# Kernel optimization log

Measured on AMD Instinct MI355X. Metric: run time of the kernel, lower is better.

The kernel has to match this reference:

```python
import jax, jax.numpy as jnp
import numpy as np

K = 1.0          # manifold curvature parameter (CustomLorentz k)
HEADS = 12
EPS = 1e-6


def add_time(space):
    """Lift space coords onto the hyperboloid: x0 = sqrt(k + ||x_s||^2)."""
    time = jnp.sqrt(K + jnp.sum(space * space, axis=-1, keepdims=True))
    return jnp.concatenate([time, space], axis=-1)


def lorentz_fc_heads(x, W):
    """LorentzFullyConnected with nheads: linear map, split space into heads,
    re-add per-head time coordinate. x: (b,n,F) -> (b,h,n,hd+1)."""
    y = x @ W                                   # (b, n, F)
    b, n, _ = y.shape
    space = y[..., 1:].reshape(b, n, HEADS, -1).transpose(0, 2, 1, 3)  # (b,h,n,hd)
    return add_time(space)


def pairwise_csqdist(q, k):
    """Lorentzian squared distance d^2(x,y) = -2k - 2<x,y>_L, pairwise."""
    inner_space = jnp.einsum('bhid,bhjd->bhij', q[..., 1:], k[..., 1:])
    inner_time = q[..., 0][..., :, None] * k[..., 0][..., None, :]
    inner = inner_space - inner_time            # Lorentz inner product
    return jnp.maximum(-2.0 * K - 2.0 * inner, EPS)


def centroid(v, w):
    """Lorentz centroid: m = w @ v; c = sqrt(k) * m / sqrt(|<m,m>_L|)."""
    m = jnp.einsum('bhij,bhjd->bhid', w, v)     # (b,h,n,hd+1)
    li = jnp.sum(m[..., 1:] ** 2, axis=-1, keepdims=True) - m[..., :1] ** 2
    denom = jnp.sqrt(jnp.maximum(jnp.abs(li), EPS))
    return jnp.sqrt(K) * m / denom


def setup_inputs() -> dict:
    key = jax.random.key(0)
    ks = jax.random.split(key, 5)
    b, n, f = 8, 1024, 769
    x_space = jax.random.normal(ks[0], (b, n, f - 1), dtype=jnp.float32) * 0.5
    x = add_time(x_space)                       # valid hyperboloid points
    init = 0.02
    Wq = jax.random.normal(ks[1], (f, f), dtype=jnp.float32) * init
    Wk = jax.random.normal(ks[2], (f, f), dtype=jnp.float32) * init
    Wv = jax.random.normal(ks[3], (f, f), dtype=jnp.float32) * init
    Wo = jax.random.normal(ks[4], (f, f), dtype=jnp.float32) * init
    return {"x": x, "Wq": Wq, "Wk": Wk, "Wv": Wv, "Wo": Wo}


def reference(x, Wq, Wk, Wv, Wo):
    b, n, _ = x.shape
    q = lorentz_fc_heads(x, Wq)                 # (b,h,n,hd+1)
    k = lorentz_fc_heads(x, Wk)
    v = lorentz_fc_heads(x, Wv)

    d2 = pairwise_csqdist(q, k)                 # (b,h,n,n)
    # score: softmax over query axis (-2) of 1/(1+log(1+d2)), then transpose
    score = jax.nn.softmax(1.0 / (1.0 + jnp.log1p(d2)), axis=-2)
    score = jnp.swapaxes(score, -1, -2)         # rows now sum to 1 over last dim

    attn = centroid(v, score)                   # (b,h,n,hd+1)

    attn_space = attn[..., 1:].transpose(0, 2, 1, 3).reshape(b, n, -1)  # (b,n,h*hd)
    attn_time = attn[..., 0].transpose(0, 2, 1)                         # (b,n,h)
    time_r = jnp.sqrt(jnp.maximum(
        jnp.sum(attn_time ** 2, axis=-1, keepdims=True) - (HEADS - 1) * K, EPS))
    merged = jnp.concatenate([time_r, attn_space], axis=-1)             # (b,n,F)

    # output LorentzFullyConnected (single-head, normalize=False, no dropout at eval)
    y = merged @ Wo
    return add_time(y[..., 1:])
```

## Files before the change

### kernel.cpp

```cpp
#include <hip/hip_runtime.h>
#include <hip/hip_bf16.h>
#include <math.h>

#define HEADS 12
#define NSEQ 1024
#define BATCH 8
#define FDIM 769
#define KP 800
#define NROWS (BATCH*NSEQ)
#define BH (BATCH*HEADS)
#define BHROWS (BH*NSEQ)

typedef __attribute__((ext_vector_type(8))) short bf16x8_t;
typedef __attribute__((ext_vector_type(4))) short bf16x4_t;
typedef __attribute__((ext_vector_type(4))) float f32x4_t;

__device__ __forceinline__ unsigned short f2bf(float f){
    unsigned u = __float_as_uint(f);
    return (unsigned short)((u + 0x7FFFu + ((u >> 16) & 1u)) >> 16);
}

__device__ __forceinline__ float fast_rcp(float x){
    return __builtin_amdgcn_rcpf(x);
}
__device__ __forceinline__ float fast_exp2(float x){
    return __builtin_amdgcn_exp2f(x);
}
__device__ __forceinline__ float fast_log2(float x){
    return __builtin_amdgcn_logf(x);
}

__global__ __launch_bounds__(256) void conv_x(const float* __restrict__ x, ushort* __restrict__ xb){
    int idx = blockIdx.x*256 + threadIdx.x;
    int r = idx / 200, c4 = (idx % 200) * 4;
    const float* row = x + (size_t)r * FDIM;
    ushort4 o;
    o.x = (c4+0 < FDIM) ? f2bf(row[c4+0]) : (ushort)0;
    o.y = (c4+1 < FDIM) ? f2bf(row[c4+1]) : (ushort)0;
    o.z = (c4+2 < FDIM) ? f2bf(row[c4+2]) : (ushort)0;
    o.w = (c4+3 < FDIM) ? f2bf(row[c4+3]) : (ushort)0;
    *(ushort4*)(xb + (size_t)r*KP + c4) = o;
}

__global__ __launch_bounds__(256) void conv_w(const float* __restrict__ Wq, const float* __restrict__ Wk,
                                              const float* __restrict__ Wv, const float* __restrict__ Wo,
                                              ushort* __restrict__ WcatT, ushort* __restrict__ WoT){
    int kt = blockIdx.x, nt = blockIdx.y, mat = blockIdx.z;
    const float* W = (mat==0)?Wq:(mat==1)?Wk:(mat==2)?Wv:Wo;
    __shared__ float T[32][33];
    int t = threadIdx.x;
    #pragma unroll
    for (int p=0; p<4; p++){
        int idx = t + p*256;
        int kk = idx>>5, nn = idx&31;
        int kp = kt*32 + kk;
        int srck;
        if (mat < 3) srck = (kp < FDIM) ? kp : -1;
        else         srck = (kp < 768) ? kp+1 : ((kp==768) ? 0 : -1);
        T[kk][nn] = (srck >= 0) ? W[(size_t)srck*FDIM + (nt*32+nn) + 1] : 0.0f;
    }
    __syncthreads();
    ushort* outp = (mat < 3) ? (WcatT + (size_t)mat*768*KP) : WoT;
    #pragma unroll
    for (int p=0; p<4; p++){
        int idx = t + p*256;
        int nl = idx>>5, kk = idx&31;
        outp[(size_t)(nt*32+nl)*KP + kt*32 + kk] = f2bf(T[kk][nl]);
    }
}

__global__ __launch_bounds__(256) void gemm_qkv(const ushort* __restrict__ A, const ushort* __restrict__ Bt,
                                                ushort* __restrict__ qkv, float* __restrict__ tbuf){
    __shared__ __align__(16) ushort As[2][128*32];
    __shared__ __align__(16) ushort Bs[2][128*32];
    const int m0 = blockIdx.x*128, n0 = blockIdx.y*128;
    const int tid = threadIdx.x, lane = tid&63, wave = tid>>6;
    const int wm = wave>>1, wn = wave&1;
    const int g = lane>>4, c = lane&15;

    f32x4_t acc[4][4];
    #pragma unroll
    for (int i=0;i<4;i++)
        #pragma unroll
        for (int j=0;j<4;j++) acc[i][j] = (f32x4_t){0.f,0.f,0.f,0.f};

    bf16x8_t ra[2], rb[2];
    auto LOADS = [&](int kt){
        int k0 = kt*32;
        #pragma unroll
        for (int p=0;p<2;p++){
            int idx = tid + p*256;
            int row = idx>>2, ch = idx&3;
            ra[p] = *(const bf16x8_t*)(A  + (size_t)(m0+row)*KP + k0 + ch*8);
            rb[p] = *(const bf16x8_t*)(Bt + (size_t)(n0+row)*KP + k0 + ch*8);
        }
    };
    auto WRITES = [&](int buf){
        #pragma unroll
        for (int p=0;p<2;p++){
            int idx = tid + p*256;
            int row = idx>>2, ch = idx&3;
            int sw = (ch ^ (row&3))*8;
            *(bf16x8_t*)&As[buf][row*32 + sw] = ra[p];
            *(bf16x8_t*)&Bs[buf][row*32 + sw] = rb[p];
        }
    };

    LOADS(0); WRITES(0); __syncthreads();
    for (int kt=0; kt<25; kt++){
        int cur = kt&1;
        if (kt+1 < 25) LOADS(kt+1);
        bf16x8_t af[4], bf[4];
        #pragma unroll
        for (int mf=0; mf<4; mf++){
            int row = wm*64 + mf*16 + c;
            af[mf] = *(const bf16x8_t*)&As[cur][row*32 + ((g ^ (row&3))*8)];
        }
        #pragma unroll
        for (int nf=0; nf<4; nf++){
            int row = wn*64 + nf*16 + c;
            bf[nf] = *(const bf16x8_t*)&Bs[cur][row*32 + ((g ^ (row&3))*8)];
        }
        #pragma unroll
        for (int mf=0; mf<4; mf++)
            #pragma unroll
            for (int nf=0; nf<4; nf++)
                acc[mf][nf] = __builtin_amdgcn_mfma_f32_16x16x32_bf16(af[mf], bf[nf], acc[mf][nf], 0,0,0);
        if (kt+1 < 25) WRITES(cur^1);
        __syncthreads();
    }

    const int nb = n0 + wn*64;
    const int matv = nb / 768;
    const int hh = (nb % 768) / 64;
    #pragma unroll
    for (int mf=0; mf<4; mf++){
        #pragma unroll
        for (int j=0; j<4; j++){
            int m = m0 + wm*64 + mf*16 + g*4 + j;
            int bb = m >> 10, ns = m & (NSEQ-1);
            size_t rowidx = ((size_t)bb*HEADS + hh)*NSEQ + ns;
            size_t sbase = (size_t)matv*((size_t)BHROWS*64) + rowidx*64;
            float sum = 0.f;
            #pragma unroll
            for (int nf=0; nf<4; nf++){
                float v = acc[mf][nf][j];
                qkv[sbase + nf*16 + c] = f2bf(v);
                sum += v*v;
            }
            sum += __shfl_xor(sum,1,64); sum += __shfl_xor(sum,2,64);
            sum += __shfl_xor(sum,4,64); sum += __shfl_xor(sum,8,64);
            if (c == 0) tbuf[(size_t)matv*BHROWS + rowidx] = sqrtf(1.0f + sum);
        }
    }
}

__global__ __launch_bounds__(256) void transpose_v(const ushort* __restrict__ vsp, ushort* __restrict__ vT){
    const int bh = blockIdx.x >> 3, it128 = blockIdx.x & 7;
    __shared__ ushort T2[64*136];
    const int tid = threadIdx.x;
    {
        int ii = tid>>1, half = tid&1;
        const ushort* src = vsp + ((size_t)bh*NSEQ + it128*128 + ii)*64 + half*32;
        bf16x8_t rr[4];
        #pragma unroll
        for (int p=0;p<4;p++) rr[p] = *(const bf16x8_t*)(src + p*8);
        #pragma unroll
        for (int p=0;p<4;p++)
            #pragma unroll
            for (int e=0;e<8;e++)
                T2[(half*32 + p*8 + e)*136 + ii] = (ushort)rr[p][e];
    }
    __syncthreads();
    {
        int dd = tid>>2, qq = tid&3;
        ushort* dst = vT + ((size_t)bh*64 + dd)*NSEQ + it128*128 + qq*32;
        #pragma unroll
        for (int p=0;p<4;p++)
            *(bf16x8_t*)(dst + p*8) = *(const bf16x8_t*)&T2[dd*136 + qq*32 + p*8];
    }
}

__global__ __launch_bounds__(256, 4) void lorentz_attn(
    const ushort* __restrict__ qsp, const ushort* __restrict__ ksp, const ushort* __restrict__ vT,
    const float* __restrict__ qtg, const float* __restrict__ ktg, const float* __restrict__ vtg,
    ushort* __restrict__ merged, float* __restrict__ ct)
{
    const int lin = blockIdx.x;
    const int bh = lin % BH;
    const int jt = lin / BH;
    const int b = bh / HEADS, h = bh % HEADS;
    const size_t rb = (size_t)bh * NSEQ;

    __shared__ __align__(16) ushort QVbuf[2][9216];
    __shared__ __align__(16) float qts[2][64];
    __shared__ __align__(16) float kts[128];

    const int tid = threadIdx.x, lane = tid&63, wave = tid>>6;
    const int g = lane>>4, c = lane&15;

    ushort* Kst = &QVbuf[0][0];

    bf16x8_t rq[2], rv[2]; float rqt = 0.f, rvt = 0.f;
    const int ii = tid>>2, qc = tid&3;
    auto LOADQV = [&](int it){
        int i0 = it*64;
        const ushort* qp = qsp + (rb + i0 + ii)*64 + qc*16;
        rq[0] = *(const bf16x8_t*)(qp);
        rq[1] = *(const bf16x8_t*)(qp + 8);
        const ushort* vp = vT + ((size_t)bh*64 + ii)*NSEQ + i0 + qc*16;
        rv[0] = *(const bf16x8_t*)(vp);
        rv[1] = *(const bf16x8_t*)(vp + 8);
        if (tid < 64) rqt = qtg[rb + i0 + tid];
        else if (tid < 128) rvt = vtg[rb + i0 + (tid-64)];
    };
    auto WRITEQV = [&](int buf){
        ushort* Qb = &QVbuf[buf][0];
        ushort* Vb = &QVbuf[buf][4096];
        *(bf16x8_t*)&Qb[ii*64 + (((2*qc  ) ^ (ii&7))*8)] = rq[0];
        *(bf16x8_t*)&Qb[ii*64 + (((2*qc+1) ^ (ii&7))*8)] = rq[1];
        #pragma unroll
        for (int s=0; s<4; s++){
            bf16x4_t sl = (s&1) ? (bf16x4_t)__builtin_shufflevector(rv[s>>1], rv[s>>1], 4,5,6,7)
                                : (bf16x4_t)__builtin_shufflevector(rv[s>>1], rv[s>>1], 0,1,2,3);
            *(bf16x4_t*)&Vb[ii*64 + ((qc*16 + s*4) ^ ((ii&7)<<2))] = sl;
        }
        if (tid < 64) qts[buf][tid] = rqt;
        else if (tid < 128) Vb[64*64 + (tid-64)] = f2bf(rvt);
    };

    LOADQV(0);
    {
        int row = tid>>1, half = tid&1;
        const ushort* kp = ksp + (rb + jt*128 + row)*64 + half*32;
        bf16x8_t kr[4];
        #pragma unroll
        for (int p=0;p<4;p++) kr[p] = *(const bf16x8_t*)(kp + p*8);
        #pragma unroll
        for (int p=0;p<4;p++){
            int c8 = half*4 + p;
            *(bf16x8_t*)&Kst[row*64 + ((c8 ^ (row&7))*8)] = kr[p];
        }
    }
    if (tid < 128) kts[tid] = ktg[rb + jt*128 + tid];
    for (int idx = tid; idx < 2*15*64; idx += 256){
        int bz = idx/(15*64), r2 = idx%(15*64);
        QVbuf[bz][4096 + (65 + (r2>>6))*64 + (r2&63)] = 0;
    }
    __syncthreads();

    bf16x8_t kfrag[2][2]; float kt2[2];
    #pragma unroll
    for (int jf=0; jf<2; jf++){
        int row = wave*32 + jf*16 + c;
        #pragma unroll
        for (int kc=0; kc<2; kc++)
            kfrag[jf][kc] = *(const bf16x8_t*)&Kst[row*64 + (((kc*4+g) ^ (row&7))*8)];
        kt2[jf] = 2.0f * kts[row];
    }
    __syncthreads();
    WRITEQV(0);
    __syncthreads();

    f32x4_t acc[2][5];
    #pragma unroll
    for (int jf=0; jf<2; jf++)
        #pragma unroll
        for (int dt=0; dt<5; dt++) acc[jf][dt] = (f32x4_t){0.f,0.f,0.f,0.f};

    for (int it=0; it<16; it++){
        int cur = it&1;
        if (it+1 < 16) LOADQV(it+1);
        ushort* Qc = &QVbuf[cur][0];
        ushort* Vc = &QVbuf[cur][4096];
        #pragma unroll
        for (int ib=0; ib<4; ib++){
            int qrow = ib*16 + c;
            bf16x8_t qf0 = *(const bf16x8_t*)&Qc[qrow*64 + (((  g) ^ (qrow&7))*8)];
            bf16x8_t qf1 = *(const bf16x8_t*)&Qc[qrow*64 + (((4+g) ^ (qrow&7))*8)];
            f32x4_t qt4 = *(const f32x4_t*)&qts[cur][ib*16 + g*4];
            bf16x4_t vf[5];
            #pragma unroll
            for (int dt=0; dt<5; dt++){
                int d = dt*16 + c;
                vf[dt] = *(const bf16x4_t*)&Vc[d*64 + ((ib*16 + g*4) ^ ((d&7)<<2))];
            }
            #pragma unroll
            for (int jf=0; jf<2; jf++){
                f32x4_t dacc = (f32x4_t){0.f,0.f,0.f,0.f};
                dacc = __builtin_amdgcn_mfma_f32_16x16x32_bf16(qf0, kfrag[jf][0], dacc, 0,0,0);
                dacc = __builtin_amdgcn_mfma_f32_16x16x32_bf16(qf1, kfrag[jf][1], dacc, 0,0,0);
                float w[4];
                #pragma unroll
                for (int r=0; r<4; r++){
                    float c0 = fmaf(qt4[r], kt2[jf], -1.0f);
                    float t  = fmaf(-2.0f, dacc[r], c0);
                    t = fmaxf(t, 1.000001f);
                    float L  = fast_log2(t);
                    float u  = fmaf(0.69314718056f, L, 1.0f);
                    w[r] = fast_exp2(fast_rcp(u) * 1.44269504089f);
                }
                __hip_bfloat162 h01 = __float22bfloat162_rn(float2{w[0], w[1]});
                __hip_bfloat162 h23 = __float22bfloat162_rn(float2{w[2], w[3]});
                union { __hip_bfloat162 h2[2]; bf16x4_t v4; } uu;
                uu.h2[0] = h01; uu.h2[1] = h23;
                bf16x4_t pa = uu.v4;
                __builtin_amdgcn_s_setprio(1);
                #pragma unroll
                for (int dt=0; dt<5; dt++)
                    acc[jf][dt] = __builtin_amdgcn_mfma_f32_16x16x16bf16_1k(pa, vf[dt], acc[jf][dt], 0,0,0);
                __builtin_amdgcn_s_setprio(0);
            }
        }
        if (it+1 < 16) WRITEQV(cur^1);
        __syncthreads();
    }

    ushort* Ms = &QVbuf[0][0];
    #pragma unroll
    for (int jf=0; jf<2; jf++){
        #pragma unroll
        for (int r=0; r<4; r++){
            float part = 0.f;
            #pragma unroll
            for (int dt=0; dt<4; dt++) part += acc[jf][dt][r]*acc[jf][dt][r];
            part += __shfl_xor(part,1,64); part += __shfl_xor(part,2,64);
            part += __shfl_xor(part,4,64); part += __shfl_xor(part,8,64);
            float tv = acc[jf][4][r];
            float tb = __shfl(tv, lane & 48, 64);
            float li = part - tb*tb;
            float f = rsqrtf(fmaxf(fabsf(li), 1e-6f));
            int jl = wave*32 + jf*16 + g*4 + r;
            #pragma unroll
            for (int dt=0; dt<4; dt++)
                Ms[jl*64 + dt*16 + c] = f2bf(acc[jf][dt][r]*f);
            if (c == 0)
                ct[((size_t)b*NSEQ + jt*128 + jl)*HEADS + h] = tb*f;
        }
    }
    __syncthreads();
    {
        int row = tid>>1, half = tid&1;
        size_t gb = ((size_t)b*NSEQ + jt*128 + row)*KP + h*64 + half*32;
        #pragma unroll
        for (int q4=0; q4<4; q4++)
            *(bf16x8_t*)(merged + gb + q4*8) = *(const bf16x8_t*)&Ms[row*64 + half*32 + q4*8];
    }
}

__global__ __launch_bounds__(256) void gemm_out_k(const ushort* __restrict__ A, const ushort* __restrict__ Bt,
                                                  float* __restrict__ out){
    __shared__ __align__(16) ushort As[2][128*32];
    __shared__ __align__(16) ushort Bs[2][128*32];
    const int m0 = blockIdx.x*128, n0 = blockIdx.y*128;
    const int tid = threadIdx.x, lane = tid&63, wave = tid>>6;
    const int wm = wave>>1, wn = wave&1;
    const int g = lane>>4, c = lane&15;

    f32x4_t acc[4][4];
    #pragma unroll
    for (int i=0;i<4;i++)
        #pragma unroll
        for (int j=0;j<4;j++) acc[i][j] = (f32x4_t){0.f,0.f,0.f,0.f};

    bf16x8_t ra[2], rb[2];
    auto LOADS = [&](int kt){
        int k0 = kt*32;
        #pragma unroll
        for (int p=0;p<2;p++){
            int idx = tid + p*256;
            int row = idx>>2, ch = idx&3;
            ra[p] = *(const bf16x8_t*)(A  + (size_t)(m0+row)*KP + k0 + ch*8);
            rb[p] = *(const bf16x8_t*)(Bt + (size_t)(n0+row)*KP + k0 + ch*8);
        }
    };
    auto WRITES = [&](int buf){
        #pragma unroll
        for (int p=0;p<2;p++){
            int idx = tid + p*256;
            int row = idx>>2, ch = idx&3;
            int sw = (ch ^ (row&3))*8;
            *(bf16x8_t*)&As[buf][row*32 + sw] = ra[p];
            *(bf16x8_t*)&Bs[buf][row*32 + sw] = rb[p];
        }
    };

    LOADS(0); WRITES(0); __syncthreads();
    for (int kt=0; kt<25; kt++){
        int cur = kt&1;
        if (kt+1 < 25) LOADS(kt+1);
        bf16x8_t af[4], bf[4];
        #pragma unroll
        for (int mf=0; mf<4; mf++){
            int row = wm*64 + mf*16 + c;
            af[mf] = *(const bf16x8_t*)&As[cur][row*32 + ((g ^ (row&3))*8)];
        }
        #pragma unroll
        for (int nf=0; nf<4; nf++){
            int row = wn*64 + nf*16 + c;
            bf[nf] = *(const bf16x8_t*)&Bs[cur][row*32 + ((g ^ (row&3))*8)];
        }
        #pragma unroll
        for (int mf=0; mf<4; mf++)
            #pragma unroll
            for (int nf=0; nf<4; nf++)
                acc[mf][nf] = __builtin_amdgcn_mfma_f32_16x16x32_bf16(af[mf], bf[nf], acc[mf][nf], 0,0,0);
        if (kt+1 < 25) WRITES(cur^1);
        __syncthreads();
    }

    #pragma unroll
    for (int mf=0; mf<4; mf++){
        #pragma unroll
        for (int j=0; j<4; j++){
            int m = m0 + wm*64 + mf*16 + g*4 + j;
            #pragma unroll
            for (int nf=0; nf<4; nf++)
                out[(size_t)m*FDIM + 1 + n0 + wn*64 + nf*16 + c] = acc[mf][nf][j];
        }
    }
}

__global__ __launch_bounds__(256) void zero_pad(ushort* __restrict__ merged){
    int idx = blockIdx.x*256 + threadIdx.x;
    int r = idx>>5, cc = idx&31;
    if (cc > 0) merged[(size_t)r*KP + 768 + cc] = 0;
}

__global__ __launch_bounds__(256) void time_r_k(const float* __restrict__ ct, ushort* __restrict__ merged){
    int r = blockIdx.x*256 + threadIdx.x;
    float s = 0.f;
    #pragma unroll
    for (int hh=0; hh<HEADS; hh++){
        float t = ct[(size_t)r*HEADS + hh];
        s = fmaf(t, t, s);
    }
    merged[(size_t)r*KP + 768] = f2bf(sqrtf(fmaxf(s - (float)(HEADS-1), 1e-6f)));
}

__global__ __launch_bounds__(256) void out_time(float* __restrict__ out)
{
    int row = blockIdx.x*4 + (threadIdx.x>>6);
    int lane = threadIdx.x & 63;
    float s = 0.f;
    #pragma unroll
    for (int l=0; l<12; l++){
        float v = out[(size_t)row*FDIM + 1 + lane + l*64];
        s = fmaf(v, v, s);
    }
    #pragma unroll
    for (int off=32; off; off>>=1) s += __shfl_down(s, off, 64);
    if (lane == 0) out[(size_t)row*FDIM] = sqrtf(1.0f + s);
}

extern "C" void kernel_launch(void* const* d_in, const int* in_sizes, int n_in,
                              void* d_out, int out_size, void* d_ws, size_t ws_size,
                              hipStream_t stream)
{
    const float* x  = (const float*)d_in[0];
    const float* Wq = (const float*)d_in[1];
    const float* Wk = (const float*)d_in[2];
    const float* Wv = (const float*)d_in[3];
    const float* Wo = (const float*)d_in[4];
    float* out = (float*)d_out;

    char* p = (char*)d_ws;
    ushort* xb     = (ushort*)p; p += (size_t)NROWS*KP*2;
    ushort* WcatT  = (ushort*)p; p += (size_t)2304*KP*2;
    ushort* WoT    = (ushort*)p; p += (size_t)768*KP*2;
    ushort* qkv    = (ushort*)p; p += (size_t)3*BHROWS*64*2;
    float*  tbuf   = (float*)p;  p += (size_t)3*BHROWS*4;
    float*  ct     = (float*)p;  p += (size_t)NROWS*HEADS*4;
    ushort* merged = (ushort*)p; p += (size_t)NROWS*KP*2;
    ushort* vT     = (ushort*)p; p += (size_t)BH*64*NSEQ*2;

    const size_t SP = (size_t)BHROWS*64;

    conv_x<<<6400, 256, 0, stream>>>(x, xb);
    conv_w<<<dim3(25,24,4), 256, 0, stream>>>(Wq, Wk, Wv, Wo, WcatT, WoT);
    gemm_qkv<<<dim3(64,18), 256, 0, stream>>>(xb, WcatT, qkv, tbuf);
    transpose_v<<<768, 256, 0, stream>>>(qkv + 2*SP, vT);
    zero_pad<<<1024, 256, 0, stream>>>(merged);
    lorentz_attn<<<768, 256, 0, stream>>>(qkv, qkv + SP, vT,
                                          tbuf, tbuf + BHROWS, tbuf + 2*BHROWS,
                                          merged, ct);
    time_r_k<<<NROWS/256, 256, 0, stream>>>(ct, merged);
    gemm_out_k<<<dim3(64,6), 256, 0, stream>>>(merged, WoT, out);
    out_time<<<NROWS/4, 256, 0, stream>>>(out);
}
```

Before: 179.2 us.

## Split attention keys across more waves, approximate log via float bits, fuse pad zeroing

The attention kernel now runs 512 threads per block, so each wave owns 16 keys instead of 32. This halves per-thread accumulators and frees registers for more resident waves. The hardware log2 is replaced by a bit-cast (Mitchell-style) log2 approximation with the constants folded in, and the lower clamp on the distance term is dropped. The separate zero_pad kernel is removed and its padding writes are merged into time_r_k. The log approximation has an absolute error of up to about 0.09 in log2, which perturbs the softmax weights and risks accuracy.

```diff
diff --git a/kernel.cpp b/kernel.cpp
--- a/kernel.cpp
+++ b/kernel.cpp
@@ -25,9 +25,6 @@
 }
 __device__ __forceinline__ float fast_exp2(float x){
     return __builtin_amdgcn_exp2f(x);
-}
-__device__ __forceinline__ float fast_log2(float x){
-    return __builtin_amdgcn_logf(x);
 }
 
 __global__ __launch_bounds__(256) void conv_x(const float* __restrict__ x, ushort* __restrict__ xb){
@@ -181,7 +178,7 @@
     }
 }
 
-__global__ __launch_bounds__(256, 4) void lorentz_attn(
+__global__ __launch_bounds__(512, 6) void lorentz_attn(
     const ushort* __restrict__ qsp, const ushort* __restrict__ ksp, const ushort* __restrict__ vT,
     const float* __restrict__ qtg, const float* __restrict__ ktg, const float* __restrict__ vtg,
     ushort* __restrict__ merged, float* __restrict__ ct)
@@ -201,72 +198,57 @@
 
     ushort* Kst = &QVbuf[0][0];
 
-    bf16x8_t rq[2], rv[2]; float rqt = 0.f, rvt = 0.f;
-    const int ii = tid>>2, qc = tid&3;
+    bf16x8_t rq, rv; float rqt = 0.f, rvt = 0.f;
+    const int srow = tid>>3, sch = tid&7;
     auto LOADQV = [&](int it){
         int i0 = it*64;
-        const ushort* qp = qsp + (rb + i0 + ii)*64 + qc*16;
-        rq[0] = *(const bf16x8_t*)(qp);
-        rq[1] = *(const bf16x8_t*)(qp + 8);
-        const ushort* vp = vT + ((size_t)bh*64 + ii)*NSEQ + i0 + qc*16;
-        rv[0] = *(const bf16x8_t*)(vp);
-        rv[1] = *(const bf16x8_t*)(vp + 8);
+        rq = *(const bf16x8_t*)(qsp + (rb + i0 + srow)*64 + sch*8);
+        rv = *(const bf16x8_t*)(vT + ((size_t)bh*64 + srow)*NSEQ + i0 + sch*8);
         if (tid < 64) rqt = qtg[rb + i0 + tid];
         else if (tid < 128) rvt = vtg[rb + i0 + (tid-64)];
     };
     auto WRITEQV = [&](int buf){
         ushort* Qb = &QVbuf[buf][0];
         ushort* Vb = &QVbuf[buf][4096];
-        *(bf16x8_t*)&Qb[ii*64 + (((2*qc  ) ^ (ii&7))*8)] = rq[0];
-        *(bf16x8_t*)&Qb[ii*64 + (((2*qc+1) ^ (ii&7))*8)] = rq[1];
-        #pragma unroll
-        for (int s=0; s<4; s++){
-            bf16x4_t sl = (s&1) ? (bf16x4_t)__builtin_shufflevector(rv[s>>1], rv[s>>1], 4,5,6,7)
-                                : (bf16x4_t)__builtin_shufflevector(rv[s>>1], rv[s>>1], 0,1,2,3);
-            *(bf16x4_t*)&Vb[ii*64 + ((qc*16 + s*4) ^ ((ii&7)<<2))] = sl;
-        }
+        *(bf16x8_t*)&Qb[srow*64 + ((sch ^ (srow&7))*8)] = rq;
+        bf16x4_t lo = __builtin_shufflevector(rv, rv, 0,1,2,3);
+        bf16x4_t hi = __builtin_shufflevector(rv, rv, 4,5,6,7);
+        *(bf16x4_t*)&Vb[srow*64 + ((sch*8    ) ^ ((srow&7)<<2))] = lo;
+        *(bf16x4_t*)&Vb[srow*64 + ((sch*8 + 4) ^ ((srow&7)<<2))] = hi;
         if (tid < 64) qts[buf][tid] = rqt;
         else if (tid < 128) Vb[64*64 + (tid-64)] = f2bf(rvt);
     };
 
     LOADQV(0);
     {
-        int row = tid>>1, half = tid&1;
-        const ushort* kp = ksp + (rb + jt*128 + row)*64 + half*32;
-        bf16x8_t kr[4];
-        #pragma unroll
-        for (int p=0;p<4;p++) kr[p] = *(const bf16x8_t*)(kp + p*8);
-        #pragma unroll
-        for (int p=0;p<4;p++){
-            int c8 = half*4 + p;
-            *(bf16x8_t*)&Kst[row*64 + ((c8 ^ (row&7))*8)] = kr[p];
-        }
+        int row = tid>>2, kc16 = tid&3;
+        const ushort* kp = ksp + (rb + jt*128 + row)*64 + kc16*16;
+        bf16x8_t k0 = *(const bf16x8_t*)(kp);
+        bf16x8_t k1 = *(const bf16x8_t*)(kp + 8);
+        *(bf16x8_t*)&Kst[row*64 + (((kc16*2  ) ^ (row&7))*8)] = k0;
+        *(bf16x8_t*)&Kst[row*64 + (((kc16*2+1) ^ (row&7))*8)] = k1;
     }
     if (tid < 128) kts[tid] = ktg[rb + jt*128 + tid];
-    for (int idx = tid; idx < 2*15*64; idx += 256){
+    for (int idx = tid; idx < 2*15*64; idx += 512){
         int bz = idx/(15*64), r2 = idx%(15*64);
         QVbuf[bz][4096 + (65 + (r2>>6))*64 + (r2&63)] = 0;
     }
     __syncthreads();
 
-    bf16x8_t kfrag[2][2]; float kt2[2];
-    #pragma unroll
-    for (int jf=0; jf<2; jf++){
-        int row = wave*32 + jf*16 + c;
-        #pragma unroll
-        for (int kc=0; kc<2; kc++)
-            kfrag[jf][kc] = *(const bf16x8_t*)&Kst[row*64 + (((kc*4+g) ^ (row&7))*8)];
-        kt2[jf] = 2.0f * kts[row];
+    bf16x8_t kfrag[2]; float kt2e;
+    {
+        int krow = wave*16 + c;
+        kfrag[0] = *(const bf16x8_t*)&Kst[krow*64 + (((  g) ^ (krow&7))*8)];
+        kfrag[1] = *(const bf16x8_t*)&Kst[krow*64 + (((4+g) ^ (krow&7))*8)];
+        kt2e = 5.43656365691809f * kts[krow];
     }
     __syncthreads();
     WRITEQV(0);
     __syncthreads();
 
-    f32x4_t acc[2][5];
-    #pragma unroll
-    for (int jf=0; jf<2; jf++)
-        #pragma unroll
-        for (int dt=0; dt<5; dt++) acc[jf][dt] = (f32x4_t){0.f,0.f,0.f,0.f};
+    f32x4_t acc[5];
+    #pragma unroll
+    for (int dt=0; dt<5; dt++) acc[dt] = (f32x4_t){0.f,0.f,0.f,0.f};
 
     for (int it=0; it<16; it++){
         int cur = it&1;
@@ -285,32 +267,27 @@
                 int d = dt*16 + c;
                 vf[dt] = *(const bf16x4_t*)&Vc[d*64 + ((ib*16 + g*4) ^ ((d&7)<<2))];
             }
-            #pragma unroll
-            for (int jf=0; jf<2; jf++){
-                f32x4_t dacc = (f32x4_t){0.f,0.f,0.f,0.f};
-                dacc = __builtin_amdgcn_mfma_f32_16x16x32_bf16(qf0, kfrag[jf][0], dacc, 0,0,0);
-                dacc = __builtin_amdgcn_mfma_f32_16x16x32_bf16(qf1, kfrag[jf][1], dacc, 0,0,0);
-                float w[4];
-                #pragma unroll
-                for (int r=0; r<4; r++){
-                    float c0 = fmaf(qt4[r], kt2[jf], -1.0f);
-                    float t  = fmaf(-2.0f, dacc[r], c0);
-                    t = fmaxf(t, 1.000001f);
-                    float L  = fast_log2(t);
-                    float u  = fmaf(0.69314718056f, L, 1.0f);
-                    w[r] = fast_exp2(fast_rcp(u) * 1.44269504089f);
-                }
-                __hip_bfloat162 h01 = __float22bfloat162_rn(float2{w[0], w[1]});
-                __hip_bfloat162 h23 = __float22bfloat162_rn(float2{w[2], w[3]});
-                union { __hip_bfloat162 h2[2]; bf16x4_t v4; } uu;
-                uu.h2[0] = h01; uu.h2[1] = h23;
-                bf16x4_t pa = uu.v4;
-                __builtin_amdgcn_s_setprio(1);
-                #pragma unroll
-                for (int dt=0; dt<5; dt++)
-                    acc[jf][dt] = __builtin_amdgcn_mfma_f32_16x16x16bf16_1k(pa, vf[dt], acc[jf][dt], 0,0,0);
-                __builtin_amdgcn_s_setprio(0);
+            f32x4_t dacc = (f32x4_t){0.f,0.f,0.f,0.f};
+            dacc = __builtin_amdgcn_mfma_f32_16x16x32_bf16(qf0, kfrag[0], dacc, 0,0,0);
+            dacc = __builtin_amdgcn_mfma_f32_16x16x32_bf16(qf1, kfrag[1], dacc, 0,0,0);
+            float w[4];
+            #pragma unroll
+            for (int r=0; r<4; r++){
+                float c0e = fmaf(qt4[r], kt2e, -2.718281828f);
+                float s   = fmaf(dacc[r], -5.43656365691809f, c0e);
+                float L   = fmaf((float)__float_as_int(s), 0x1p-23f, -126.9570f);
+                w[r] = fast_exp2(fast_rcp(L) * 2.08136898f);
             }
+            __hip_bfloat162 h01 = __float22bfloat162_rn(float2{w[0], w[1]});
+            __hip_bfloat162 h23 = __float22bfloat162_rn(float2{w[2], w[3]});
+            union { __hip_bfloat162 h2[2]; bf16x4_t v4; } uu;
+            uu.h2[0] = h01; uu.h2[1] = h23;
+            bf16x4_t pa = uu.v4;
+            __builtin_amdgcn_s_setprio(1);
+            #pragma unroll
+            for (int dt=0; dt<5; dt++)
+                acc[dt] = __builtin_amdgcn_mfma_f32_16x16x16bf16_1k(pa, vf[dt], acc[dt], 0,0,0);
+            __builtin_amdgcn_s_setprio(0);
         }
         if (it+1 < 16) WRITEQV(cur^1);
         __syncthreads();
@@ -318,33 +295,29 @@
 
     ushort* Ms = &QVbuf[0][0];
     #pragma unroll
-    for (int jf=0; jf<2; jf++){
-        #pragma unroll
-        for (int r=0; r<4; r++){
-            float part = 0.f;
-            #pragma unroll
-            for (int dt=0; dt<4; dt++) part += acc[jf][dt][r]*acc[jf][dt][r];
-            part += __shfl_xor(part,1,64); part += __shfl_xor(part,2,64);
-            part += __shfl_xor(part,4,64); part += __shfl_xor(part,8,64);
-            float tv = acc[jf][4][r];
-            float tb = __shfl(tv, lane & 48, 64);
-            float li = part - tb*tb;
-            float f = rsqrtf(fmaxf(fabsf(li), 1e-6f));
-            int jl = wave*32 + jf*16 + g*4 + r;
-            #pragma unroll
-            for (int dt=0; dt<4; dt++)
-                Ms[jl*64 + dt*16 + c] = f2bf(acc[jf][dt][r]*f);
-            if (c == 0)
-                ct[((size_t)b*NSEQ + jt*128 + jl)*HEADS + h] = tb*f;
-        }
+    for (int r=0; r<4; r++){
+        float part = 0.f;
+        #pragma unroll
+        for (int dt=0; dt<4; dt++) part += acc[dt][r]*acc[dt][r];
+        part += __shfl_xor(part,1,64); part += __shfl_xor(part,2,64);
+        part += __shfl_xor(part,4,64); part += __shfl_xor(part,8,64);
+        float tv = acc[4][r];
+        float tb = __shfl(tv, lane & 48, 64);
+        float li = part - tb*tb;
+        float f = rsqrtf(fmaxf(fabsf(li), 1e-6f));
+        int jl = wave*16 + g*4 + r;
+        #pragma unroll
+        for (int dt=0; dt<4; dt++)
+            Ms[jl*64 + dt*16 + c] = f2bf(acc[dt][r]*f);
+        if (c == 0)
+            ct[((size_t)b*NSEQ + jt*128 + jl)*HEADS + h] = tb*f;
     }
     __syncthreads();
     {
-        int row = tid>>1, half = tid&1;
-        size_t gb = ((size_t)b*NSEQ + jt*128 + row)*KP + h*64 + half*32;
-        #pragma unroll
-        for (int q4=0; q4<4; q4++)
-            *(bf16x8_t*)(merged + gb + q4*8) = *(const bf16x8_t*)&Ms[row*64 + half*32 + q4*8];
+        int row = tid>>2, q16 = tid&3;
+        size_t gb = ((size_t)b*NSEQ + jt*128 + row)*KP + h*64 + q16*16;
+        *(bf16x8_t*)(merged + gb)     = *(const bf16x8_t*)&Ms[row*64 + q16*16];
+        *(bf16x8_t*)(merged + gb + 8) = *(const bf16x8_t*)&Ms[row*64 + q16*16 + 8];
     }
 }
 
@@ -421,12 +394,6 @@
     }
 }
 
-__global__ __launch_bounds__(256) void zero_pad(ushort* __restrict__ merged){
-    int idx = blockIdx.x*256 + threadIdx.x;
-    int r = idx>>5, cc = idx&31;
-    if (cc > 0) merged[(size_t)r*KP + 768 + cc] = 0;
-}
-
 __global__ __launch_bounds__(256) void time_r_k(const float* __restrict__ ct, ushort* __restrict__ merged){
     int r = blockIdx.x*256 + threadIdx.x;
     float s = 0.f;
@@ -435,7 +402,14 @@
         float t = ct[(size_t)r*HEADS + hh];
         s = fmaf(t, t, s);
     }
-    merged[(size_t)r*KP + 768] = f2bf(sqrtf(fmaxf(s - (float)(HEADS-1), 1e-6f)));
+    bf16x8_t z = (bf16x8_t){0,0,0,0,0,0,0,0};
+    bf16x8_t z0 = z;
+    z0[0] = (short)f2bf(sqrtf(fmaxf(s - (float)(HEADS-1), 1e-6f)));
+    ushort* dst = merged + (size_t)r*KP + 768;
+    *(bf16x8_t*)(dst)      = z0;
+    *(bf16x8_t*)(dst + 8)  = z;
+    *(bf16x8_t*)(dst + 16) = z;
+    *(bf16x8_t*)(dst + 24) = z;
 }
 
 __global__ __launch_bounds__(256) void out_time(float* __restrict__ out)
@@ -480,8 +454,7 @@
     conv_w<<<dim3(25,24,4), 256, 0, stream>>>(Wq, Wk, Wv, Wo, WcatT, WoT);
     gemm_qkv<<<dim3(64,18), 256, 0, stream>>>(xb, WcatT, qkv, tbuf);
     transpose_v<<<768, 256, 0, stream>>>(qkv + 2*SP, vT);
-    zero_pad<<<1024, 256, 0, stream>>>(merged);
-    lorentz_attn<<<768, 256, 0, stream>>>(qkv, qkv + SP, vT,
+    lorentz_attn<<<768, 512, 0, stream>>>(qkv, qkv + SP, vT,
                                           tbuf, tbuf + BHROWS, tbuf + 2*BHROWS,
                                           merged, ct);
     time_r_k<<<NROWS/256, 256, 0, stream>>>(ct, merged);
```

Measured after the change: 172.8 us. -3.6%, faster.

## Use bit-trick log approximation, wider PV MFMA, and fold zero_pad into time_r

Applied to the files above, without the earlier changes.

Swaps the log2 in the score transform for an integer-reinterpretation log approximation with rescaled constants, which removes one transcendental per score. Two query sub-blocks are now processed per iteration so the P·V product can use the 16x16x32 MFMA with 8-wide fragments; this needed a new V tile swizzle and a permuted time-row layout. The separate zero_pad launch is removed and time_r_k writes the padded row with vector stores. Launch bounds drop to 3 waves per SIMD to leave room for more registers. The bit-trick log is a coarse approximation, so accuracy on the score path may suffer.

```diff
diff --git a/kernel.cpp b/kernel.cpp
--- a/kernel.cpp
+++ b/kernel.cpp
@@ -25,9 +25,6 @@
 }
 __device__ __forceinline__ float fast_exp2(float x){
     return __builtin_amdgcn_exp2f(x);
-}
-__device__ __forceinline__ float fast_log2(float x){
-    return __builtin_amdgcn_logf(x);
 }
 
 __global__ __launch_bounds__(256) void conv_x(const float* __restrict__ x, ushort* __restrict__ xb){
@@ -181,7 +178,7 @@
     }
 }
 
-__global__ __launch_bounds__(256, 4) void lorentz_attn(
+__global__ __launch_bounds__(256, 3) void lorentz_attn(
     const ushort* __restrict__ qsp, const ushort* __restrict__ ksp, const ushort* __restrict__ vT,
     const float* __restrict__ qtg, const float* __restrict__ ktg, const float* __restrict__ vtg,
     ushort* __restrict__ merged, float* __restrict__ ct)
@@ -202,13 +199,13 @@
     ushort* Kst = &QVbuf[0][0];
 
     bf16x8_t rq[2], rv[2]; float rqt = 0.f, rvt = 0.f;
-    const int ii = tid>>2, qc = tid&3;
+    const int sr = tid>>2, sch = tid&3;
     auto LOADQV = [&](int it){
         int i0 = it*64;
-        const ushort* qp = qsp + (rb + i0 + ii)*64 + qc*16;
+        const ushort* qp = qsp + (rb + i0 + sr)*64 + sch*16;
         rq[0] = *(const bf16x8_t*)(qp);
         rq[1] = *(const bf16x8_t*)(qp + 8);
-        const ushort* vp = vT + ((size_t)bh*64 + ii)*NSEQ + i0 + qc*16;
+        const ushort* vp = vT + ((size_t)bh*64 + sr)*NSEQ + i0 + sch*16;
         rv[0] = *(const bf16x8_t*)(vp);
         rv[1] = *(const bf16x8_t*)(vp + 8);
         if (tid < 64) rqt = qtg[rb + i0 + tid];
@@ -217,29 +214,33 @@
     auto WRITEQV = [&](int buf){
         ushort* Qb = &QVbuf[buf][0];
         ushort* Vb = &QVbuf[buf][4096];
-        *(bf16x8_t*)&Qb[ii*64 + (((2*qc  ) ^ (ii&7))*8)] = rq[0];
-        *(bf16x8_t*)&Qb[ii*64 + (((2*qc+1) ^ (ii&7))*8)] = rq[1];
+        *(bf16x8_t*)&Qb[sr*64 + (((2*sch  ) ^ (sr&7))*8)] = rq[0];
+        *(bf16x8_t*)&Qb[sr*64 + (((2*sch+1) ^ (sr&7))*8)] = rq[1];
+        int pbase = (sch>>1)*32 + (sch&1)*4;
+        int sx = (sr&7)*8;
         #pragma unroll
         for (int s=0; s<4; s++){
             bf16x4_t sl = (s&1) ? (bf16x4_t)__builtin_shufflevector(rv[s>>1], rv[s>>1], 4,5,6,7)
                                 : (bf16x4_t)__builtin_shufflevector(rv[s>>1], rv[s>>1], 0,1,2,3);
-            *(bf16x4_t*)&Vb[ii*64 + ((qc*16 + s*4) ^ ((ii&7)<<2))] = sl;
+            *(bf16x4_t*)&Vb[sr*64 + ((pbase + 8*s) ^ sx)] = sl;
         }
         if (tid < 64) qts[buf][tid] = rqt;
-        else if (tid < 128) Vb[64*64 + (tid-64)] = f2bf(rvt);
+        else if (tid < 128){
+            int i = tid - 64;
+            int p = 32*(i>>5) + 8*((i>>2)&3) + 4*((i>>4)&1) + (i&3);
+            Vb[64*64 + p] = f2bf(rvt);
+        }
     };
 
     LOADQV(0);
     {
         int row = tid>>1, half = tid&1;
         const ushort* kp = ksp + (rb + jt*128 + row)*64 + half*32;
-        bf16x8_t kr[4];
-        #pragma unroll
-        for (int p=0;p<4;p++) kr[p] = *(const bf16x8_t*)(kp + p*8);
-        #pragma unroll
-        for (int p=0;p<4;p++){
+        #pragma unroll
+        for (int p=0; p<4; p++){
+            bf16x8_t kr = *(const bf16x8_t*)(kp + p*8);
             int c8 = half*4 + p;
-            *(bf16x8_t*)&Kst[row*64 + ((c8 ^ (row&7))*8)] = kr[p];
+            *(bf16x8_t*)&Kst[row*64 + ((c8 ^ (row&7))*8)] = kr;
         }
     }
     if (tid < 128) kts[tid] = ktg[rb + jt*128 + tid];
@@ -249,14 +250,13 @@
     }
     __syncthreads();
 
-    bf16x8_t kfrag[2][2]; float kt2[2];
+    bf16x8_t kfrag[2][2]; float kt2e[2];
     #pragma unroll
     for (int jf=0; jf<2; jf++){
-        int row = wave*32 + jf*16 + c;
-        #pragma unroll
-        for (int kc=0; kc<2; kc++)
-            kfrag[jf][kc] = *(const bf16x8_t*)&Kst[row*64 + (((kc*4+g) ^ (row&7))*8)];
-        kt2[jf] = 2.0f * kts[row];
+        int krow = wave*32 + jf*16 + c;
+        kfrag[jf][0] = *(const bf16x8_t*)&Kst[krow*64 + (((  g) ^ (krow&7))*8)];
+        kfrag[jf][1] = *(const bf16x8_t*)&Kst[krow*64 + (((4+g) ^ (krow&7))*8)];
+        kt2e[jf] = 5.43656365691809f * kts[krow];
     }
     __syncthreads();
     WRITEQV(0);
@@ -274,41 +274,52 @@
         ushort* Qc = &QVbuf[cur][0];
         ushort* Vc = &QVbuf[cur][4096];
         #pragma unroll
-        for (int ib=0; ib<4; ib++){
-            int qrow = ib*16 + c;
-            bf16x8_t qf0 = *(const bf16x8_t*)&Qc[qrow*64 + (((  g) ^ (qrow&7))*8)];
-            bf16x8_t qf1 = *(const bf16x8_t*)&Qc[qrow*64 + (((4+g) ^ (qrow&7))*8)];
-            f32x4_t qt4 = *(const f32x4_t*)&qts[cur][ib*16 + g*4];
-            bf16x4_t vf[5];
+        for (int ib2=0; ib2<2; ib2++){
+            bf16x8_t qf[2][2];
+            #pragma unroll
+            for (int t=0; t<2; t++){
+                int qrow = ib2*32 + t*16 + c;
+                qf[t][0] = *(const bf16x8_t*)&Qc[qrow*64 + (((  g) ^ (qrow&7))*8)];
+                qf[t][1] = *(const bf16x8_t*)&Qc[qrow*64 + (((4+g) ^ (qrow&7))*8)];
+            }
+            f32x4_t qt0 = *(const f32x4_t*)&qts[cur][ib2*32 + g*4];
+            f32x4_t qt1 = *(const f32x4_t*)&qts[cur][ib2*32 + 16 + g*4];
+            bf16x8_t vf[5];
             #pragma unroll
             for (int dt=0; dt<5; dt++){
                 int d = dt*16 + c;
-                vf[dt] = *(const bf16x4_t*)&Vc[d*64 + ((ib*16 + g*4) ^ ((d&7)<<2))];
+                vf[dt] = *(const bf16x8_t*)&Vc[d*64 + ((ib2*32 + g*8) ^ ((d&7)*8))];
             }
             #pragma unroll
             for (int jf=0; jf<2; jf++){
-                f32x4_t dacc = (f32x4_t){0.f,0.f,0.f,0.f};
-                dacc = __builtin_amdgcn_mfma_f32_16x16x32_bf16(qf0, kfrag[jf][0], dacc, 0,0,0);
-                dacc = __builtin_amdgcn_mfma_f32_16x16x32_bf16(qf1, kfrag[jf][1], dacc, 0,0,0);
-                float w[4];
+                f32x4_t d0 = (f32x4_t){0.f,0.f,0.f,0.f};
+                f32x4_t d1 = (f32x4_t){0.f,0.f,0.f,0.f};
+                d0 = __builtin_amdgcn_mfma_f32_16x16x32_bf16(qf[0][0], kfrag[jf][0], d0, 0,0,0);
+                d0 = __builtin_amdgcn_mfma_f32_16x16x32_bf16(qf[0][1], kfrag[jf][1], d0, 0,0,0);
+                d1 = __builtin_amdgcn_mfma_f32_16x16x32_bf16(qf[1][0], kfrag[jf][0], d1, 0,0,0);
+                d1 = __builtin_amdgcn_mfma_f32_16x16x32_bf16(qf[1][1], kfrag[jf][1], d1, 0,0,0);
+                float w0[4], w1[4];
                 #pragma unroll
                 for (int r=0; r<4; r++){
-                    float c0 = fmaf(qt4[r], kt2[jf], -1.0f);
-                    float t  = fmaf(-2.0f, dacc[r], c0);
-                    t = fmaxf(t, 1.000001f);
-                    float L  = fast_log2(t);
-                    float u  = fmaf(0.69314718056f, L, 1.0f);
-                    w[r] = fast_exp2(fast_rcp(u) * 1.44269504089f);
+                    float c0 = fmaf(qt0[r], kt2e[jf], -2.718281828f);
+                    float s0 = fmaf(d0[r], -5.43656365691809f, c0);
+                    float L0 = fmaf((float)__float_as_int(s0), 0x1p-23f, -126.9570f);
+                    w0[r] = fast_exp2(fast_rcp(L0) * 2.08136898f);
+                    float c1 = fmaf(qt1[r], kt2e[jf], -2.718281828f);
+                    float s1 = fmaf(d1[r], -5.43656365691809f, c1);
+                    float L1 = fmaf((float)__float_as_int(s1), 0x1p-23f, -126.9570f);
+                    w1[r] = fast_exp2(fast_rcp(L1) * 2.08136898f);
                 }
-                __hip_bfloat162 h01 = __float22bfloat162_rn(float2{w[0], w[1]});
-                __hip_bfloat162 h23 = __float22bfloat162_rn(float2{w[2], w[3]});
-                union { __hip_bfloat162 h2[2]; bf16x4_t v4; } uu;
-                uu.h2[0] = h01; uu.h2[1] = h23;
-                bf16x4_t pa = uu.v4;
+                union { __hip_bfloat162 h2[4]; bf16x8_t v8; } uu;
+                uu.h2[0] = __float22bfloat162_rn(float2{w0[0], w0[1]});
+                uu.h2[1] = __float22bfloat162_rn(float2{w0[2], w0[3]});
+                uu.h2[2] = __float22bfloat162_rn(float2{w1[0], w1[1]});
+                uu.h2[3] = __float22bfloat162_rn(float2{w1[2], w1[3]});
+                bf16x8_t pa = uu.v8;
                 __builtin_amdgcn_s_setprio(1);
                 #pragma unroll
                 for (int dt=0; dt<5; dt++)
-                    acc[jf][dt] = __builtin_amdgcn_mfma_f32_16x16x16bf16_1k(pa, vf[dt], acc[jf][dt], 0,0,0);
+                    acc[jf][dt] = __builtin_amdgcn_mfma_f32_16x16x32_bf16(pa, vf[dt], acc[jf][dt], 0,0,0);
                 __builtin_amdgcn_s_setprio(0);
             }
         }
@@ -344,7 +355,7 @@
         size_t gb = ((size_t)b*NSEQ + jt*128 + row)*KP + h*64 + half*32;
         #pragma unroll
         for (int q4=0; q4<4; q4++)
-            *(bf16x8_t*)(merged + gb + q4*8) = *(const bf16x8_t*)&Ms[row*64 + half*32 + q4*8];
+            *(bf16x8_t*)(merged + gb + half*0 + q4*8) = *(const bf16x8_t*)&Ms[row*64 + half*32 + q4*8];
     }
 }
 
@@ -421,12 +432,6 @@
     }
 }
 
-__global__ __launch_bounds__(256) void zero_pad(ushort* __restrict__ merged){
-    int idx = blockIdx.x*256 + threadIdx.x;
-    int r = idx>>5, cc = idx&31;
-    if (cc > 0) merged[(size_t)r*KP + 768 + cc] = 0;
-}
-
 __global__ __launch_bounds__(256) void time_r_k(const float* __restrict__ ct, ushort* __restrict__ merged){
     int r = blockIdx.x*256 + threadIdx.x;
     float s = 0.f;
@@ -435,7 +440,14 @@
         float t = ct[(size_t)r*HEADS + hh];
         s = fmaf(t, t, s);
     }
-    merged[(size_t)r*KP + 768] = f2bf(sqrtf(fmaxf(s - (float)(HEADS-1), 1e-6f)));
+    bf16x8_t z = (bf16x8_t){0,0,0,0,0,0,0,0};
+    bf16x8_t z0 = z;
+    z0[0] = (short)f2bf(sqrtf(fmaxf(s - (float)(HEADS-1), 1e-6f)));
+    ushort* dst = merged + (size_t)r*KP + 768;
+    *(bf16x8_t*)(dst)      = z0;
+    *(bf16x8_t*)(dst + 8)  = z;
+    *(bf16x8_t*)(dst + 16) = z;
+    *(bf16x8_t*)(dst + 24) = z;
 }
 
 __global__ __launch_bounds__(256) void out_time(float* __restrict__ out)
@@ -480,7 +492,6 @@
     conv_w<<<dim3(25,24,4), 256, 0, stream>>>(Wq, Wk, Wv, Wo, WcatT, WoT);
     gemm_qkv<<<dim3(64,18), 256, 0, stream>>>(xb, WcatT, qkv, tbuf);
     transpose_v<<<768, 256, 0, stream>>>(qkv + 2*SP, vT);
-    zero_pad<<<1024, 256, 0, stream>>>(merged);
     lorentz_attn<<<768, 256, 0, stream>>>(qkv, qkv + SP, vT,
                                           tbuf, tbuf + BHROWS, tbuf + 2*BHROWS,
                                           merged, ct);
```

New measurement: 163.2 us. 8.9% less time.
